# Kernel optimization log

Hardware: AMD Instinct MI355X
Metric: run time of the kernel (lower is better)

The kernel has to match this reference:

```python
import jax, jax.numpy as jnp
import numpy as np

L = 3        # num_layers
H = 512      # hidden_dim
T = 64       # traj_len
LAT = 128    # latent_dim
COND = 128   # condition_dim
B = 2048     # batch


def setup_inputs() -> dict:
    key = jax.random.key(0)
    ks = jax.random.split(key, 8)
    s = 0.05
    d = LAT + COND
    return {
        "z": jax.random.normal(ks[0], (B, LAT), dtype=jnp.float32),
        "condition": jax.random.normal(ks[1], (B, COND), dtype=jnp.float32),
        # hidden_proj: Linear(latent+cond -> L*H)
        "hp_W": jax.random.normal(ks[2], (L * H, d), dtype=jnp.float32) * s,
        "hp_b": jnp.zeros((L * H,), dtype=jnp.float32),
        # GRU weights (PyTorch layout, gate order r,z,n)
        "W_ih0": jax.random.normal(ks[3], (3 * H, 2), dtype=jnp.float32) * s,
        "W_ih_rest": jax.random.normal(ks[4], (L - 1, 3 * H, H), dtype=jnp.float32) * s,
        "W_hh": jax.random.normal(ks[5], (L, 3 * H, H), dtype=jnp.float32) * s,
        "b_ih": jnp.zeros((L, 3 * H), dtype=jnp.float32),
        "b_hh": jnp.zeros((L, 3 * H), dtype=jnp.float32),
        # per-step output MLPs: Linear(H,H) -> ReLU -> Linear(H,2)
        "W1": jax.random.normal(ks[6], (T, H, H), dtype=jnp.float32) * s,
        "b1": jnp.zeros((T, H), dtype=jnp.float32),
        "W2": jax.random.normal(ks[7], (T, H, 2), dtype=jnp.float32) * s,
        "b2": jnp.zeros((T, 2), dtype=jnp.float32),
    }


def _gru_cell(x, h, W_ih, W_hh, b_ih, b_hh):
    # PyTorch GRU cell: gates in order (r, z, n)
    gi = x @ W_ih.T + b_ih        # (B, 3H)
    gh = h @ W_hh.T + b_hh        # (B, 3H)
    ir, iz, inn = jnp.split(gi, 3, axis=-1)
    hr, hz, hn = jnp.split(gh, 3, axis=-1)
    r = jax.nn.sigmoid(ir + hr)
    zg = jax.nn.sigmoid(iz + hz)
    n = jnp.tanh(inn + r * hn)
    return (1.0 - zg) * n + zg * h


def reference(z, condition, hp_W, hp_b, W_ih0, W_ih_rest, W_hh, b_ih, b_hh, W1, b1, W2, b2):
    Bsz = z.shape[0]
    combined = jnp.concatenate([z, condition], axis=1)            # (B, LAT+COND)
    h0 = (combined @ hp_W.T + hp_b).reshape(Bsz, L, H).transpose(1, 0, 2)  # (L, B, H)
    pos0 = jnp.zeros((Bsz, 2), dtype=z.dtype)

    def step(carry, ws):
        h, pos = carry                     # h: (L,B,H), pos: (B,2) = current_pos
        w1, bb1, w2, bb2 = ws              # this step's MLP weights
        x = pos
        new_h = []
        for l in range(L):                 # fixed small layer loop
            Wih = W_ih0 if l == 0 else W_ih_rest[l - 1]
            hl = _gru_cell(x, h[l], Wih, W_hh[l], b_ih[l], b_hh[l])
            new_h.append(hl)
            x = hl
        delta = jax.nn.relu(x @ w1 + bb1) @ w2 + bb2   # (B,2); dropout is identity at eval
        new_pos = pos + delta              # cumulative sum of deltas
        return (jnp.stack(new_h), new_pos), new_pos

    (_, _), traj = jax.lax.scan(step, (h0, pos0), (W1, b1, W2, b2))
    return traj.transpose(1, 0, 2)         # (B, T, 2)
```

## Files before the change

kernel.cpp:

```cpp
#include <hip/hip_runtime.h>
#include <hip/hip_bf16.h>


#define H 512
#define T_STEPS 64
#define BATCH 2048
#define H3 1536
#define D_IN 256
#define NSTRIP 8

typedef __bf16 bf16x8 __attribute__((ext_vector_type(8)));
typedef float f32x4 __attribute__((ext_vector_type(4)));
typedef unsigned short ushort8v __attribute__((ext_vector_type(8)));
typedef unsigned short ushort4v __attribute__((ext_vector_type(4)));

typedef const __attribute__((address_space(1))) unsigned int* gp1_t;
typedef __attribute__((address_space(3))) unsigned int* lp3_t;

__device__ inline void gload16(const unsigned short* g, unsigned short* l) {
    __builtin_amdgcn_global_load_lds((gp1_t)g, (lp3_t)l, 16, 0, 0);
}

__device__ inline unsigned short f2bf(float f) {
    union { float f; unsigned int u; } v{f};
    unsigned int r = v.u + 0x7fffu + ((v.u >> 16) & 1u);
    return (unsigned short)(r >> 16);
}
__device__ inline float bf2f(unsigned short u) {
    union { unsigned int u; float f; } v;
    v.u = ((unsigned int)u) << 16;
    return v.f;
}
__device__ inline float sigmoidf_(float x) { return 1.f / (1.f + expf(-x)); }

__device__ inline int soff(int r, int ko) {
    return r * 32 + ((ko ^ ((r >> 1) & 3)) << 3);
}

__device__ inline void stage128(const unsigned short* src, int ld, int k0,
                                unsigned short* lds) {
    const int wid = threadIdx.x >> 6, lane = threadIdx.x & 63;
#pragma unroll
    for (int i = 0; i < 2; ++i) {
        int off = i * 4096 + wid * 1024 + lane * 16;
        int row = off >> 6;
        int c = (off >> 4) & 3;
        int cs = c ^ ((row >> 1) & 3);
        gload16(src + (size_t)row * ld + k0 + cs * 8,
                lds + ((i * 4096 + wid * 1024) >> 1));
    }
}

__device__ inline void gcore(const unsigned short* A0, int lda,
                             const unsigned short* W0, int K,
                             unsigned short (*As)[4096], unsigned short (*Ws)[4096],
                             f32x4 (&acc)[4][4]) {
    const int lane = threadIdx.x & 63, wid = threadIdx.x >> 6;
    const int wr = wid >> 1, wc = wid & 1;
    const int r16 = lane & 15, ko = lane >> 4;
#pragma unroll
    for (int i = 0; i < 4; ++i)
#pragma unroll
        for (int j = 0; j < 4; ++j) acc[i][j] = (f32x4)0.f;
    int aoff[4], boff[4];
#pragma unroll
    for (int i = 0; i < 4; ++i) {
        aoff[i] = soff(wr * 64 + i * 16 + r16, ko);
        boff[i] = soff(wc * 64 + i * 16 + r16, ko);
    }
    stage128(A0, lda, 0, As[0]);
    stage128(W0, K, 0, Ws[0]);
    __syncthreads();
    int cur = 0;
    for (int k0 = 0; k0 < K; k0 += 32) {
        const bool more = (k0 + 32) < K;
        if (more) {
            stage128(A0, lda, k0 + 32, As[cur ^ 1]);
            stage128(W0, K, k0 + 32, Ws[cur ^ 1]);
        }
        bf16x8 a[4], b[4];
#pragma unroll
        for (int i = 0; i < 4; ++i) a[i] = *(const bf16x8*)&As[cur][aoff[i]];
#pragma unroll
        for (int i = 0; i < 4; ++i) b[i] = *(const bf16x8*)&Ws[cur][boff[i]];
#pragma unroll
        for (int mi = 0; mi < 4; ++mi)
#pragma unroll
            for (int ni = 0; ni < 4; ++ni)
                acc[mi][ni] = __builtin_amdgcn_mfma_f32_16x16x32_bf16(
                    a[mi], b[ni], acc[mi][ni], 0, 0, 0);
        if (more) {
            __syncthreads();
            cur ^= 1;
        }
    }
}

__device__ inline void epilogue_f32(f32x4 (&acc)[4][4], float* C, int ldc,
                                    const float* bias, unsigned short* Cbf,
                                    int brow, int bcol) {
    const int lane = threadIdx.x & 63, wid = threadIdx.x >> 6;
    const int wr = wid >> 1, wc = wid & 1, r16 = lane & 15;
    const int crow0 = brow + wr * 64 + (lane >> 4) * 4;
    const int ccol0 = bcol + wc * 64 + r16;
#pragma unroll
    for (int mi = 0; mi < 4; ++mi)
#pragma unroll
        for (int ni = 0; ni < 4; ++ni) {
            int col = ccol0 + ni * 16;
            float bv = bias ? bias[col] : 0.f;
#pragma unroll
            for (int j = 0; j < 4; ++j) {
                int row = crow0 + mi * 16 + j;
                float v = acc[mi][ni][j] + bv;
                C[(size_t)row * ldc + col] = v;
                if (Cbf) Cbf[(size_t)row * ldc + col] = f2bf(v);
            }
        }
}

__device__ inline void epilogue_bf(f32x4 (&acc)[4][4], unsigned short* C, int ldc,
                                   int brow, int bcol) {
    const int lane = threadIdx.x & 63, wid = threadIdx.x >> 6;
    const int wr = wid >> 1, wc = wid & 1, r16 = lane & 15;
    const int crow0 = brow + wr * 64 + (lane >> 4) * 4;
    const int ccol0 = bcol + wc * 64 + r16;
#pragma unroll
    for (int mi = 0; mi < 4; ++mi)
#pragma unroll
        for (int ni = 0; ni < 4; ++ni) {
            int col = ccol0 + ni * 16;
#pragma unroll
            for (int j = 0; j < 4; ++j) {
                int row = crow0 + mi * 16 + j;
                C[(size_t)row * ldc + col] = f2bf(acc[mi][ni][j]);
            }
        }
}

__device__ inline void epilogue_mlp(f32x4 (&acc)[4][4], const float* b1t,
                                    const float* W2t, float* partials, int brow,
                                    int bcol) {
    const int lane = threadIdx.x & 63, wid = threadIdx.x >> 6;
    const int wr = wid >> 1, wc = wid & 1, r16 = lane & 15;
    const int crow0 = brow + wr * 64 + (lane >> 4) * 4;
    const int ccol0 = bcol + wc * 64 + r16;
    const int strip = (bcol >> 7) * 2 + wc;
    float d0[4][4], d1[4][4];
#pragma unroll
    for (int mi = 0; mi < 4; ++mi)
#pragma unroll
        for (int j = 0; j < 4; ++j) { d0[mi][j] = 0.f; d1[mi][j] = 0.f; }
#pragma unroll
    for (int ni = 0; ni < 4; ++ni) {
        int col = ccol0 + ni * 16;
        float bv = b1t[col];
        float w20 = W2t[col * 2 + 0], w21 = W2t[col * 2 + 1];
#pragma unroll
        for (int mi = 0; mi < 4; ++mi)
#pragma unroll
            for (int j = 0; j < 4; ++j) {
                float hv = fmaxf(acc[mi][ni][j] + bv, 0.f);
                d0[mi][j] += hv * w20;
                d1[mi][j] += hv * w21;
            }
    }
#pragma unroll
    for (int m = 1; m < 16; m <<= 1)
#pragma unroll
        for (int mi = 0; mi < 4; ++mi)
#pragma unroll
            for (int j = 0; j < 4; ++j) {
                d0[mi][j] += __shfl_xor(d0[mi][j], m);
                d1[mi][j] += __shfl_xor(d1[mi][j], m);
            }
    if (r16 == 0) {
#pragma unroll
        for (int mi = 0; mi < 4; ++mi)
#pragma unroll
            for (int j = 0; j < 4; ++j) {
                int row = crow0 + mi * 16 + j;
                float2 v = make_float2(d0[mi][j], d1[mi][j]);
                *(float2*)&partials[((size_t)strip * BATCH + row) * 2] = v;
            }
    }
}

__global__ __launch_bounds__(256) void k_init(const unsigned short* comb,
                                              const unsigned short* hpW, float* h,
                                              unsigned short* h_bf,
                                              const float* hp_b) {
    __shared__ unsigned short As[2][4096], Ws[2][4096];
    f32x4 acc[4][4];
    int bid = blockIdx.x;
    int brow = (bid / 12) * 128, bcol = (bid % 12) * 128;
    gcore(comb + (size_t)brow * D_IN, D_IN, hpW + (size_t)bcol * D_IN, D_IN, As, Ws,
          acc);
    epilogue_f32(acc, h, H3, hp_b, h_bf, brow, bcol);
}

__global__ __launch_bounds__(256) void k_gh3(const unsigned short* h_bf,
                                             const unsigned short* Whh,
                                             unsigned short* gh0, unsigned short* gh1,
                                             unsigned short* gh2) {
    __shared__ unsigned short As[2][4096], Ws[2][4096];
    f32x4 acc[4][4];
    int bid = blockIdx.x;
    int g = bid / 192, r = bid % 192;
    int brow = (r / 12) * 128, bcol = (r % 12) * 128;
    unsigned short* C = (g == 0) ? gh0 : (g == 1 ? gh1 : gh2);
    gcore(h_bf + g * H + (size_t)brow * H3, H3,
          Whh + (size_t)g * H3 * H + (size_t)bcol * H, H, As, Ws, acc);
    epilogue_bf(acc, C, H3, brow, bcol);
}

__global__ __launch_bounds__(256) void k_dual(const unsigned short* A,
                                              const unsigned short* W0,
                                              unsigned short* C0,
                                              const unsigned short* W1,
                                              unsigned short* C1, int skip2) {
    __shared__ unsigned short As[2][4096], Ws[2][4096];
    f32x4 acc[4][4];
    int bid = blockIdx.x;
    int half = bid >= 192;
    if (half && skip2) return;
    int r = bid - half * 192;
    int brow = (r / 12) * 128, bcol = (r % 12) * 128;
    const unsigned short* W = half ? W1 : W0;
    unsigned short* C = half ? C1 : C0;
    gcore(A + (size_t)brow * H3, H3, W + (size_t)bcol * H, H, As, Ws, acc);
    epilogue_bf(acc, C, H3, brow, bcol);
}

__global__ __launch_bounds__(256) void k_mlp_gh(const unsigned short* A,
                                                const unsigned short* W1Tt,
                                                const float* b1t, const float* W2t,
                                                float* partials,
                                                const unsigned short* Whh2,
                                                unsigned short* gh2, int skip2) {
    __shared__ unsigned short As[2][4096], Ws[2][4096];
    f32x4 acc[4][4];
    int bid = blockIdx.x;
    if (bid < 64) {
        int brow = (bid >> 2) * 128, bcol = (bid & 3) * 128;
        gcore(A + (size_t)brow * H3, H3, W1Tt + (size_t)bcol * H, H, As, Ws, acc);
        epilogue_mlp(acc, b1t, W2t, partials, brow, bcol);
    } else {
        if (skip2) return;
        int r = bid - 64;
        int brow = (r / 12) * 128, bcol = (r % 12) * 128;
        gcore(A + (size_t)brow * H3, H3, Whh2 + (size_t)bcol * H, H, As, Ws, acc);
        epilogue_bf(acc, gh2, H3, brow, bcol);
    }
}

__global__ __launch_bounds__(256) void k_ew0(const unsigned short* gh0, float* h,
                                             unsigned short* h_bf,
                                             const float* W_ih0, const float* b_ih,
                                             const float* b_hh, float* pos,
                                             const float* partials, const float* b2,
                                             float* out, int t) {
    __shared__ float posS[2][2];
    const int tid = threadIdx.x, bid = blockIdx.x;
    if (tid < 2) {
        int b = bid * 2 + tid;
        float p0 = pos[b * 2 + 0], p1 = pos[b * 2 + 1];
        if (t > 0) {
            float s0 = 0.f, s1 = 0.f;
#pragma unroll
            for (int s = 0; s < NSTRIP; ++s) {
                float2 v = *(const float2*)&partials[((size_t)s * BATCH + b) * 2];
                s0 += v.x; s1 += v.y;
            }
            p0 += s0 + b2[(t - 1) * 2 + 0];
            p1 += s1 + b2[(t - 1) * 2 + 1];
            pos[b * 2 + 0] = p0;
            pos[b * 2 + 1] = p1;
            out[((size_t)b * T_STEPS + (t - 1)) * 2 + 0] = p0;
            out[((size_t)b * T_STEPS + (t - 1)) * 2 + 1] = p1;
        }
        posS[tid][0] = p0;
        posS[tid][1] = p1;
    }
    __syncthreads();
    const int lrow = tid >> 7, j0 = (tid & 127) * 4;
    const int b = bid * 2 + lrow;
    const size_t rb = (size_t)b * H3;
    const float px = posS[lrow][0], py = posS[lrow][1];
    ushort4v g0 = *(const ushort4v*)&gh0[rb + j0];
    ushort4v g1 = *(const ushort4v*)&gh0[rb + 512 + j0];
    ushort4v g2 = *(const ushort4v*)&gh0[rb + 1024 + j0];
    float4 h4 = *(const float4*)&h[rb + j0];
    float hv[4] = {h4.x, h4.y, h4.z, h4.w};
    float4 ho;
    ushort4v hbo;
#pragma unroll
    for (int k = 0; k < 4; ++k) {
        int j = j0 + k;
        float gi_r = px * W_ih0[j * 2 + 0] + py * W_ih0[j * 2 + 1] + b_ih[j];
        float gi_z = px * W_ih0[(512 + j) * 2 + 0] + py * W_ih0[(512 + j) * 2 + 1] +
                     b_ih[512 + j];
        float gi_n = px * W_ih0[(1024 + j) * 2 + 0] + py * W_ih0[(1024 + j) * 2 + 1] +
                     b_ih[1024 + j];
        float r = sigmoidf_(gi_r + bf2f(g0[k]) + b_hh[j]);
        float zg = sigmoidf_(gi_z + bf2f(g1[k]) + b_hh[512 + j]);
        float n = tanhf(gi_n + r * (bf2f(g2[k]) + b_hh[1024 + j]));
        float nh = (1.f - zg) * n + zg * hv[k];
        ((float*)&ho)[k] = nh;
        hbo[k] = f2bf(nh);
    }
    *(float4*)&h[rb + j0] = ho;
    *(ushort4v*)&h_bf[rb + j0] = hbo;
}

__global__ __launch_bounds__(256) void k_ewl(const unsigned short* gi,
                                             const unsigned short* gh, float* h,
                                             unsigned short* h_bf,
                                             const float* b_ihl, const float* b_hhl,
                                             int colOff) {
    const int tid = threadIdx.x, bid = blockIdx.x;
    const int lrow = tid >> 7, j0 = (tid & 127) * 4;
    const int b = bid * 2 + lrow;
    const size_t rb = (size_t)b * H3;
    ushort4v ir4 = *(const ushort4v*)&gi[rb + j0];
    ushort4v iz4 = *(const ushort4v*)&gi[rb + 512 + j0];
    ushort4v in4 = *(const ushort4v*)&gi[rb + 1024 + j0];
    ushort4v hr4 = *(const ushort4v*)&gh[rb + j0];
    ushort4v hz4 = *(const ushort4v*)&gh[rb + 512 + j0];
    ushort4v hn4 = *(const ushort4v*)&gh[rb + 1024 + j0];
    float4 bir = *(const float4*)&b_ihl[j0];
    float4 biz = *(const float4*)&b_ihl[512 + j0];
    float4 bin = *(const float4*)&b_ihl[1024 + j0];
    float4 bhr = *(const float4*)&b_hhl[j0];
    float4 bhz = *(const float4*)&b_hhl[512 + j0];
    float4 bhn = *(const float4*)&b_hhl[1024 + j0];
    float4 h4 = *(const float4*)&h[rb + colOff + j0];
    float bi_r[4] = {bir.x, bir.y, bir.z, bir.w};
    float bi_z[4] = {biz.x, biz.y, biz.z, biz.w};
    float bi_n[4] = {bin.x, bin.y, bin.z, bin.w};
    float bh_r[4] = {bhr.x, bhr.y, bhr.z, bhr.w};
    float bh_z[4] = {bhz.x, bhz.y, bhz.z, bhz.w};
    float bh_n[4] = {bhn.x, bhn.y, bhn.z, bhn.w};
    float hv[4] = {h4.x, h4.y, h4.z, h4.w};
    float4 ho;
    ushort4v hbo;
#pragma unroll
    for (int k = 0; k < 4; ++k) {
        float r = sigmoidf_(bf2f(ir4[k]) + bi_r[k] + bf2f(hr4[k]) + bh_r[k]);
        float zg = sigmoidf_(bf2f(iz4[k]) + bi_z[k] + bf2f(hz4[k]) + bh_z[k]);
        float n = tanhf(bf2f(in4[k]) + bi_n[k] + r * (bf2f(hn4[k]) + bh_n[k]));
        float nh = (1.f - zg) * n + zg * hv[k];
        ((float*)&ho)[k] = nh;
        hbo[k] = f2bf(nh);
    }
    *(float4*)&h[rb + colOff + j0] = ho;
    *(ushort4v*)&h_bf[rb + colOff + j0] = hbo;
}

__global__ __launch_bounds__(256) void k_posfin(const float* partials, float* pos,
                                                const float* b2, float* out) {
    int b = blockIdx.x * 256 + threadIdx.x;
    float s0 = 0.f, s1 = 0.f;
#pragma unroll
    for (int s = 0; s < NSTRIP; ++s) {
        float2 v = *(const float2*)&partials[((size_t)s * BATCH + b) * 2];
        s0 += v.x; s1 += v.y;
    }
    float p0 = pos[b * 2 + 0] + s0 + b2[63 * 2 + 0];
    float p1 = pos[b * 2 + 1] + s1 + b2[63 * 2 + 1];
    out[((size_t)b * T_STEPS + 63) * 2 + 0] = p0;
    out[((size_t)b * T_STEPS + 63) * 2 + 1] = p1;
}

__global__ __launch_bounds__(256) void k_comb(const float* z, const float* cond,
                                              unsigned short* comb, float* pos) {
    int idx = blockIdx.x * 256 + threadIdx.x;
    int b = idx >> 8, k = idx & 255;
    float v = (k < 128) ? z[b * 128 + k] : cond[b * 128 + (k - 128)];
    comb[idx] = f2bf(v);
    if (idx < BATCH * 2) pos[idx] = 0.f;
}

__global__ __launch_bounds__(256) void k_conv(const float* in, unsigned short* out) {
    size_t i = ((size_t)blockIdx.x * 256 + threadIdx.x) * 8;
    float4 v0 = *(const float4*)(in + i);
    float4 v1 = *(const float4*)(in + i + 4);
    ushort8v p;
    p[0] = f2bf(v0.x); p[1] = f2bf(v0.y); p[2] = f2bf(v0.z); p[3] = f2bf(v0.w);
    p[4] = f2bf(v1.x); p[5] = f2bf(v1.y); p[6] = f2bf(v1.z); p[7] = f2bf(v1.w);
    *(ushort8v*)(out + i) = p;
}

__global__ __launch_bounds__(256) void k_trw1(const float* W1, unsigned short* W1T) {
    __shared__ float tile[32][33];
    int t = blockIdx.z;
    int n0 = blockIdx.x * 32, k0 = blockIdx.y * 32;
    int tx = threadIdx.x & 31, ty = threadIdx.x >> 5;
#pragma unroll
    for (int j = 0; j < 4; ++j)
        tile[ty + 8 * j][tx] = W1[((size_t)t * 512 + k0 + ty + 8 * j) * 512 + n0 + tx];
    __syncthreads();
#pragma unroll
    for (int j = 0; j < 4; ++j)
        W1T[((size_t)t * 512 + n0 + ty + 8 * j) * 512 + k0 + tx] =
            f2bf(tile[tx][ty + 8 * j]);
}

extern "C" void kernel_launch(void* const* d_in, const int* in_sizes, int n_in,
                              void* d_out, int out_size, void* d_ws, size_t ws_size,
                              hipStream_t stream) {
    const float* z = (const float*)d_in[0];
    const float* cond = (const float*)d_in[1];
    const float* hp_W = (const float*)d_in[2];
    const float* hp_b = (const float*)d_in[3];
    const float* W_ih0 = (const float*)d_in[4];
    const float* W_ihr = (const float*)d_in[5];
    const float* W_hh = (const float*)d_in[6];
    const float* b_ih = (const float*)d_in[7];
    const float* b_hh = (const float*)d_in[8];
    const float* W1 = (const float*)d_in[9];
    const float* b1 = (const float*)d_in[10];
    const float* W2 = (const float*)d_in[11];
    const float* b2 = (const float*)d_in[12];
    float* out = (float*)d_out;

    char* w = (char*)d_ws;
    float* pos = (float*)w;           w += (size_t)BATCH * 2 * 4;
    float* partials = (float*)w;      w += (size_t)NSTRIP * BATCH * 2 * 4;
    float* h = (float*)w;             w += (size_t)BATCH * H3 * 4;
    unsigned short* gi = (unsigned short*)w;      w += (size_t)BATCH * H3 * 2;
    unsigned short* gh0 = (unsigned short*)w;     w += (size_t)BATCH * H3 * 2;
    unsigned short* gh1 = (unsigned short*)w;     w += (size_t)BATCH * H3 * 2;
    unsigned short* gh2 = (unsigned short*)w;     w += (size_t)BATCH * H3 * 2;
    unsigned short* h_bf = (unsigned short*)w;    w += (size_t)BATCH * H3 * 2;
    unsigned short* comb_bf = (unsigned short*)w; w += (size_t)BATCH * D_IN * 2;
    unsigned short* hpW_bf = (unsigned short*)w;  w += (size_t)H3 * D_IN * 2;
    unsigned short* Whh_bf = (unsigned short*)w;  w += (size_t)3 * H3 * H * 2;
    unsigned short* Wihr_bf = (unsigned short*)w; w += (size_t)2 * H3 * H * 2;
    unsigned short* W1T_bf = (unsigned short*)w;  w += (size_t)T_STEPS * H * H * 2;

    k_comb<<<dim3((BATCH * D_IN) / 256), dim3(256), 0, stream>>>(z, cond, comb_bf, pos);
    k_conv<<<dim3((H3 * D_IN) / 2048), dim3(256), 0, stream>>>(hp_W, hpW_bf);
    k_conv<<<dim3((3 * H3 * H) / 2048), dim3(256), 0, stream>>>(W_hh, Whh_bf);
    k_conv<<<dim3((2 * H3 * H) / 2048), dim3(256), 0, stream>>>(W_ihr, Wihr_bf);
    k_trw1<<<dim3(16, 16, T_STEPS), dim3(256), 0, stream>>>(W1, W1T_bf);
    k_init<<<dim3(192), dim3(256), 0, stream>>>(comb_bf, hpW_bf, h, h_bf, hp_b);
    k_gh3<<<dim3(576), dim3(256), 0, stream>>>(h_bf, Whh_bf, gh0, gh1, gh2);

    for (int t = 0; t < T_STEPS; ++t) {
        int last = (t == T_STEPS - 1) ? 1 : 0;
        k_ew0<<<dim3(1024), dim3(256), 0, stream>>>(gh0, h, h_bf, W_ih0, b_ih, b_hh,
                                                    pos, partials, b2, out, t);
        k_dual<<<dim3(384), dim3(256), 0, stream>>>(h_bf, Wihr_bf, gi, Whh_bf, gh0,
                                                    last);
        k_ewl<<<dim3(1024), dim3(256), 0, stream>>>(gi, gh1, h, h_bf, b_ih + H3,
                                                    b_hh + H3, H);
        k_dual<<<dim3(384), dim3(256), 0, stream>>>(
            h_bf + H, Wihr_bf + (size_t)H3 * H, gi, Whh_bf + (size_t)H3 * H, gh1,
            last);
        k_ewl<<<dim3(1024), dim3(256), 0, stream>>>(gi, gh2, h, h_bf, b_ih + 2 * H3,
                                                    b_hh + 2 * H3, 2 * H);
        k_mlp_gh<<<dim3(256), dim3(256), 0, stream>>>(
            h_bf + 2 * H, W1T_bf + (size_t)t * H * H, b1 + (size_t)t * H,
            W2 + (size_t)t * H * 2, partials, Whh_bf + (size_t)2 * H3 * H, gh2, last);
    }
    k_posfin<<<dim3(8), dim3(256), 0, stream>>>(partials, pos, b2, out);
}
```

Before: 4.186 ms.

## Rebalance recurrent gh GEMM tiles across the three per-step GEMM launches

```diff
diff --git a/kernel.cpp b/kernel.cpp
--- a/kernel.cpp
+++ b/kernel.cpp
@@ -183,6 +183,42 @@
                 float2 v = make_float2(d0[mi][j], d1[mi][j]);
                 *(float2*)&partials[((size_t)strip * BATCH + row) * 2] = v;
             }
+    }
+}
+
+struct TD {
+    const unsigned short* A;
+    const unsigned short* W;
+    unsigned short* C;
+    int t0;
+};
+
+__global__ __launch_bounds__(256) void k_tri(TD d0, TD d1, TD d2, int n0, int n1,
+                                             int mlp0, const float* b1t,
+                                             const float* W2t, float* partials,
+                                             int skipGh) {
+    __shared__ unsigned short As[2][4096], Ws[2][4096];
+    f32x4 acc[4][4];
+    const int bid = blockIdx.x;
+    TD d;
+    int r, isMlp = 0;
+    if (bid < n0) {
+        d = d0; r = d0.t0 + bid; isMlp = mlp0;
+    } else if (bid < n0 + n1) {
+        if (skipGh) return;
+        d = d1; r = d1.t0 + (bid - n0);
+    } else {
+        if (skipGh) return;
+        d = d2; r = d2.t0 + (bid - n0 - n1);
+    }
+    if (isMlp) {
+        int brow = (r >> 2) * 128, bcol = (r & 3) * 128;
+        gcore(d.A + (size_t)brow * H3, H3, d.W + (size_t)bcol * H, H, As, Ws, acc);
+        epilogue_mlp(acc, b1t, W2t, partials, brow, bcol);
+    } else {
+        int brow = (r / 12) * 128, bcol = (r % 12) * 128;
+        gcore(d.A + (size_t)brow * H3, H3, d.W + (size_t)bcol * H, H, As, Ws, acc);
+        epilogue_bf(acc, d.C, H3, brow, bcol);
     }
 }
 
@@ -212,46 +248,6 @@
     gcore(h_bf + g * H + (size_t)brow * H3, H3,
           Whh + (size_t)g * H3 * H + (size_t)bcol * H, H, As, Ws, acc);
     epilogue_bf(acc, C, H3, brow, bcol);
-}
-
-__global__ __launch_bounds__(256) void k_dual(const unsigned short* A,
-                                              const unsigned short* W0,
-                                              unsigned short* C0,
-                                              const unsigned short* W1,
-                                              unsigned short* C1, int skip2) {
-    __shared__ unsigned short As[2][4096], Ws[2][4096];
-    f32x4 acc[4][4];
-    int bid = blockIdx.x;
-    int half = bid >= 192;
-    if (half && skip2) return;
-    int r = bid - half * 192;
-    int brow = (r / 12) * 128, bcol = (r % 12) * 128;
-    const unsigned short* W = half ? W1 : W0;
-    unsigned short* C = half ? C1 : C0;
-    gcore(A + (size_t)brow * H3, H3, W + (size_t)bcol * H, H, As, Ws, acc);
-    epilogue_bf(acc, C, H3, brow, bcol);
-}
-
-__global__ __launch_bounds__(256) void k_mlp_gh(const unsigned short* A,
-                                                const unsigned short* W1Tt,
-                                                const float* b1t, const float* W2t,
-                                                float* partials,
-                                                const unsigned short* Whh2,
-                                                unsigned short* gh2, int skip2) {
-    __shared__ unsigned short As[2][4096], Ws[2][4096];
-    f32x4 acc[4][4];
-    int bid = blockIdx.x;
-    if (bid < 64) {
-        int brow = (bid >> 2) * 128, bcol = (bid & 3) * 128;
-        gcore(A + (size_t)brow * H3, H3, W1Tt + (size_t)bcol * H, H, As, Ws, acc);
-        epilogue_mlp(acc, b1t, W2t, partials, brow, bcol);
-    } else {
-        if (skip2) return;
-        int r = bid - 64;
-        int brow = (r / 12) * 128, bcol = (r % 12) * 128;
-        gcore(A + (size_t)brow * H3, H3, Whh2 + (size_t)bcol * H, H, As, Ws, acc);
-        epilogue_bf(acc, gh2, H3, brow, bcol);
-    }
 }
 
 __global__ __launch_bounds__(256) void k_ew0(const unsigned short* gh0, float* h,
@@ -447,22 +443,44 @@
     k_init<<<dim3(192), dim3(256), 0, stream>>>(comb_bf, hpW_bf, h, h_bf, hp_b);
     k_gh3<<<dim3(576), dim3(256), 0, stream>>>(h_bf, Whh_bf, gh0, gh1, gh2);
 
+    const unsigned short* Whh0 = Whh_bf;
+    const unsigned short* Whh1 = Whh_bf + (size_t)H3 * H;
+    const unsigned short* Whh2 = Whh_bf + (size_t)2 * H3 * H;
+    const unsigned short* Wihr0 = Wihr_bf;
+    const unsigned short* Wihr1 = Wihr_bf + (size_t)H3 * H;
+
     for (int t = 0; t < T_STEPS; ++t) {
         int last = (t == T_STEPS - 1) ? 1 : 0;
         k_ew0<<<dim3(1024), dim3(256), 0, stream>>>(gh0, h, h_bf, W_ih0, b_ih, b_hh,
                                                     pos, partials, b2, out, t);
-        k_dual<<<dim3(384), dim3(256), 0, stream>>>(h_bf, Wihr_bf, gi, Whh_bf, gh0,
-                                                    last);
+        {
+            TD s0{h_bf, Wihr0, gi, 0};
+            TD s1{h_bf, Whh0, gh0, 0};
+            TD s2{nullptr, nullptr, nullptr, 0};
+            k_tri<<<dim3(256), dim3(256), 0, stream>>>(s0, s1, s2, 192, 64, 0,
+                                                       nullptr, nullptr, nullptr,
+                                                       last);
+        }
         k_ewl<<<dim3(1024), dim3(256), 0, stream>>>(gi, gh1, h, h_bf, b_ih + H3,
                                                     b_hh + H3, H);
-        k_dual<<<dim3(384), dim3(256), 0, stream>>>(
-            h_bf + H, Wihr_bf + (size_t)H3 * H, gi, Whh_bf + (size_t)H3 * H, gh1,
-            last);
+        {
+            TD s0{h_bf + H, Wihr1, gi, 0};
+            TD s1{h_bf + H, Whh1, gh1, 0};
+            TD s2{h_bf, Whh0, gh0, 64};
+            k_tri<<<dim3(448), dim3(256), 0, stream>>>(s0, s1, s2, 192, 128, 0,
+                                                       nullptr, nullptr, nullptr,
+                                                       last);
+        }
         k_ewl<<<dim3(1024), dim3(256), 0, stream>>>(gi, gh2, h, h_bf, b_ih + 2 * H3,
                                                     b_hh + 2 * H3, 2 * H);
-        k_mlp_gh<<<dim3(256), dim3(256), 0, stream>>>(
-            h_bf + 2 * H, W1T_bf + (size_t)t * H * H, b1 + (size_t)t * H,
-            W2 + (size_t)t * H * 2, partials, Whh_bf + (size_t)2 * H3 * H, gh2, last);
+        {
+            TD s0{h_bf + 2 * H, W1T_bf + (size_t)t * H * H, nullptr, 0};
+            TD s1{h_bf + 2 * H, Whh2, gh2, 0};
+            TD s2{h_bf + H, Whh1, gh1, 128};
+            k_tri<<<dim3(320), dim3(256), 0, stream>>>(
+                s0, s1, s2, 64, 192, 1, b1 + (size_t)t * H,
+                W2 + (size_t)t * H * 2, partials, last);
+        }
     }
     k_posfin<<<dim3(8), dim3(256), 0, stream>>>(partials, pos, b2, out);
 }
```

Result: no change. 4.238 ms (+1.2%).

## Triple-buffer GEMM LDS staging with vmcnt waits and a single barrier per step

Applied to the files above, without the earlier changes.

```diff
diff --git a/kernel.cpp b/kernel.cpp
--- a/kernel.cpp
+++ b/kernel.cpp
@@ -21,6 +21,12 @@
     __builtin_amdgcn_global_load_lds((gp1_t)g, (lp3_t)l, 16, 0, 0);
 }
 
+template <int N>
+__device__ inline void waitv() {
+    asm volatile("s_waitcnt vmcnt(%0)" ::"n"(N) : "memory");
+    __builtin_amdgcn_sched_barrier(0);
+}
+
 __device__ inline unsigned short f2bf(float f) {
     union { float f; unsigned int u; } v{f};
     unsigned int r = v.u + 0x7fffu + ((v.u >> 16) & 1u);
@@ -37,8 +43,8 @@
     return r * 32 + ((ko ^ ((r >> 1) & 3)) << 3);
 }
 
-__device__ inline void stage128(const unsigned short* src, int ld, int k0,
-                                unsigned short* lds) {
+__device__ inline void stage32(const unsigned short* src, int ld, int k0,
+                               unsigned short* lds) {
     const int wid = threadIdx.x >> 6, lane = threadIdx.x & 63;
 #pragma unroll
     for (int i = 0; i < 2; ++i) {
@@ -51,6 +57,7 @@
     }
 }
 
+template <int NSTEP>
 __device__ inline void gcore(const unsigned short* A0, int lda,
                              const unsigned short* W0, int K,
                              unsigned short (*As)[4096], unsigned short (*Ws)[4096],
@@ -68,32 +75,33 @@
         aoff[i] = soff(wr * 64 + i * 16 + r16, ko);
         boff[i] = soff(wc * 64 + i * 16 + r16, ko);
     }
-    stage128(A0, lda, 0, As[0]);
-    stage128(W0, K, 0, Ws[0]);
-    __syncthreads();
-    int cur = 0;
-    for (int k0 = 0; k0 < K; k0 += 32) {
-        const bool more = (k0 + 32) < K;
-        if (more) {
-            stage128(A0, lda, k0 + 32, As[cur ^ 1]);
-            stage128(W0, K, k0 + 32, Ws[cur ^ 1]);
+    stage32(A0, lda, 0, As[0]);
+    stage32(W0, K, 0, Ws[0]);
+    stage32(A0, lda, 32, As[1]);
+    stage32(W0, K, 32, Ws[1]);
+#pragma unroll
+    for (int i = 0; i < NSTEP; ++i) {
+        if (i == NSTEP - 1) waitv<0>(); else waitv<4>();
+        __builtin_amdgcn_s_barrier();
+        if (i + 2 < NSTEP) {
+            stage32(A0, lda, (i + 2) * 32, As[(i + 2) % 3]);
+            stage32(W0, K, (i + 2) * 32, Ws[(i + 2) % 3]);
         }
+        const unsigned short* Ac = As[i % 3];
+        const unsigned short* Wc = Ws[i % 3];
         bf16x8 a[4], b[4];
 #pragma unroll
-        for (int i = 0; i < 4; ++i) a[i] = *(const bf16x8*)&As[cur][aoff[i]];
-#pragma unroll
-        for (int i = 0; i < 4; ++i) b[i] = *(const bf16x8*)&Ws[cur][boff[i]];
+        for (int j = 0; j < 4; ++j) a[j] = *(const bf16x8*)&Ac[aoff[j]];
+#pragma unroll
+        for (int j = 0; j < 4; ++j) b[j] = *(const bf16x8*)&Wc[boff[j]];
 #pragma unroll
         for (int mi = 0; mi < 4; ++mi)
 #pragma unroll
             for (int ni = 0; ni < 4; ++ni)
                 acc[mi][ni] = __builtin_amdgcn_mfma_f32_16x16x32_bf16(
                     a[mi], b[ni], acc[mi][ni], 0, 0, 0);
-        if (more) {
-            __syncthreads();
-            cur ^= 1;
-        }
-    }
+    }
+    __syncthreads();
 }
 
 __device__ inline void epilogue_f32(f32x4 (&acc)[4][4], float* C, int ldc,
@@ -190,12 +198,12 @@
                                               const unsigned short* hpW, float* h,
                                               unsigned short* h_bf,
                                               const float* hp_b) {
-    __shared__ unsigned short As[2][4096], Ws[2][4096];
+    __shared__ unsigned short As[3][4096], Ws[3][4096];
     f32x4 acc[4][4];
     int bid = blockIdx.x;
     int brow = (bid / 12) * 128, bcol = (bid % 12) * 128;
-    gcore(comb + (size_t)brow * D_IN, D_IN, hpW + (size_t)bcol * D_IN, D_IN, As, Ws,
-          acc);
+    gcore<8>(comb + (size_t)brow * D_IN, D_IN, hpW + (size_t)bcol * D_IN, D_IN, As,
+             Ws, acc);
     epilogue_f32(acc, h, H3, hp_b, h_bf, brow, bcol);
 }
 
@@ -203,14 +211,14 @@
                                              const unsigned short* Whh,
                                              unsigned short* gh0, unsigned short* gh1,
                                              unsigned short* gh2) {
-    __shared__ unsigned short As[2][4096], Ws[2][4096];
+    __shared__ unsigned short As[3][4096], Ws[3][4096];
     f32x4 acc[4][4];
     int bid = blockIdx.x;
     int g = bid / 192, r = bid % 192;
     int brow = (r / 12) * 128, bcol = (r % 12) * 128;
     unsigned short* C = (g == 0) ? gh0 : (g == 1 ? gh1 : gh2);
-    gcore(h_bf + g * H + (size_t)brow * H3, H3,
-          Whh + (size_t)g * H3 * H + (size_t)bcol * H, H, As, Ws, acc);
+    gcore<16>(h_bf + g * H + (size_t)brow * H3, H3,
+              Whh + (size_t)g * H3 * H + (size_t)bcol * H, H, As, Ws, acc);
     epilogue_bf(acc, C, H3, brow, bcol);
 }
 
@@ -219,7 +227,7 @@
                                               unsigned short* C0,
                                               const unsigned short* W1,
                                               unsigned short* C1, int skip2) {
-    __shared__ unsigned short As[2][4096], Ws[2][4096];
+    __shared__ unsigned short As[3][4096], Ws[3][4096];
     f32x4 acc[4][4];
     int bid = blockIdx.x;
     int half = bid >= 192;
@@ -228,7 +236,7 @@
     int brow = (r / 12) * 128, bcol = (r % 12) * 128;
     const unsigned short* W = half ? W1 : W0;
     unsigned short* C = half ? C1 : C0;
-    gcore(A + (size_t)brow * H3, H3, W + (size_t)bcol * H, H, As, Ws, acc);
+    gcore<16>(A + (size_t)brow * H3, H3, W + (size_t)bcol * H, H, As, Ws, acc);
     epilogue_bf(acc, C, H3, brow, bcol);
 }
 
@@ -238,18 +246,20 @@
                                                 float* partials,
                                                 const unsigned short* Whh2,
                                                 unsigned short* gh2, int skip2) {
-    __shared__ unsigned short As[2][4096], Ws[2][4096];
+    __shared__ unsigned short As[3][4096], Ws[3][4096];
     f32x4 acc[4][4];
     int bid = blockIdx.x;
     if (bid < 64) {
         int brow = (bid >> 2) * 128, bcol = (bid & 3) * 128;
-        gcore(A + (size_t)brow * H3, H3, W1Tt + (size_t)bcol * H, H, As, Ws, acc);
+        gcore<16>(A + (size_t)brow * H3, H3, W1Tt + (size_t)bcol * H, H, As, Ws,
+                  acc);
         epilogue_mlp(acc, b1t, W2t, partials, brow, bcol);
     } else {
         if (skip2) return;
         int r = bid - 64;
         int brow = (r / 12) * 128, bcol = (r % 12) * 128;
-        gcore(A + (size_t)brow * H3, H3, Whh2 + (size_t)bcol * H, H, As, Ws, acc);
+        gcore<16>(A + (size_t)brow * H3, H3, Whh2 + (size_t)bcol * H, H, As, Ws,
+                  acc);
         epilogue_bf(acc, gh2, H3, brow, bcol);
     }
 }
```

Measured after the change: 4.247 ms. About the same (+1.5%).
